# Performance work log

Measured on AMD Instinct MI355X. Metric: run time of the kernel, lower is better.

Reference implementation:

```python
import jax, jax.numpy as jnp
import numpy as np

NUM_NODES = 12
NUM_EDGES = 30
OUT_CH = 32
HID = 192
B = 8192
FEAT = 2 * (NUM_NODES - 1)            # 22
N = B * NUM_NODES                      # 98304 nodes
E = B * NUM_EDGES                      # 245760 edges
OUT_SPACE = NUM_NODES ** 2 - NUM_NODES # 132


def setup_inputs() -> dict:
    key = jax.random.key(0)
    ks = jax.random.split(key, 16)
    def p(k, shape, fan):
        return jax.random.normal(k, shape, dtype=jnp.float32) / np.float32(np.sqrt(fan))
    return {
        "x": jax.random.normal(ks[0], (N, FEAT), dtype=jnp.float32),
        "edge_attr": jax.random.normal(ks[1], (E, NUM_EDGES), dtype=jnp.float32),
        "edge_index": jax.random.randint(ks[2], (2, E), 0, N, dtype=jnp.int64) if jax.config.jax_enable_x64 else jax.random.randint(ks[2], (2, E), 0, N, dtype=jnp.int32),
        "mlp1_w1": p(ks[3], (NUM_EDGES, HID), NUM_EDGES),
        "mlp1_b1": jnp.zeros((HID,), jnp.float32),
        "mlp1_w2": p(ks[4], (HID, FEAT * OUT_CH), HID),
        "mlp1_b2": jnp.zeros((FEAT * OUT_CH,), jnp.float32),
        "root1": p(ks[5], (FEAT, OUT_CH), FEAT),
        "bias1": jnp.zeros((OUT_CH,), jnp.float32),
        "lin1_w": p(ks[6], (NUM_NODES * OUT_CH, 96), NUM_NODES * OUT_CH),
        "lin1_b": jnp.zeros((96,), jnp.float32),
        "lin2_w": p(ks[7], (96, 48), 96),
        "lin2_b": jnp.zeros((48,), jnp.float32),
        "lin3_w": p(ks[8], (48, OUT_SPACE), 48),
        "lin3_b": jnp.zeros((OUT_SPACE,), jnp.float32),
    }


def reference(x, edge_attr, edge_index, mlp1_w1, mlp1_b1, mlp1_w2, mlp1_b2,
              root1, bias1, lin1_w, lin1_b, lin2_w, lin2_b, lin3_w, lin3_b):
    src, dst = edge_index[0], edge_index[1]
    # Edge-MLP ('Understanding'): produces a [FEAT, OUT_CH] weight per edge
    h = jax.nn.relu(edge_attr @ mlp1_w1 + mlp1_b1)               # [E, HID]
    W = (h @ mlp1_w2 + mlp1_b2).reshape(-1, FEAT, OUT_CH)        # [E, 22, 32]
    # NNConv: gather source features, per-edge matmul, scatter-add to dst
    msg = jnp.einsum('ec,eco->eo', x[src], W)                    # [E, 32]
    agg = jax.ops.segment_sum(msg, dst, num_segments=x.shape[0]) # [N, 32]
    g = jax.nn.relu(x @ root1 + agg + bias1)                     # conv1 + ReLU
    # Dense head
    g = g.reshape(-1, NUM_NODES * OUT_CH)                        # [B, 384]
    g = jax.nn.relu(g @ lin1_w + lin1_b)
    g = jax.nn.relu(g @ lin2_w + lin2_b)
    g = jax.nn.relu(g @ lin3_w + lin3_b)                         # [B, 132]
    return g
```

## Files before the change

kernel.cpp:

```cpp
#include <hip/hip_runtime.h>
#include <hip/hip_bf16.h>

typedef short s8v __attribute__((ext_vector_type(8)));
typedef float f4v __attribute__((ext_vector_type(4)));

#define MFMA16(A,B,C) __builtin_amdgcn_mfma_f32_16x16x32_bf16((A),(B),(C),0,0,0)

#define E_TOT 245760
#define N_TOT 98304

__device__ __forceinline__ unsigned short f2bf(float f) {
    unsigned u = __builtin_bit_cast(unsigned, f);
    u += 0x7fffu + ((u >> 16) & 1u);
    return (unsigned short)(u >> 16);
}
__device__ __forceinline__ float bflo(unsigned u) {
    return __builtin_bit_cast(float, u << 16);
}
__device__ __forceinline__ float bfhi(unsigned u) {
    return __builtin_bit_cast(float, u & 0xffff0000u);
}
__device__ __forceinline__ void gload_lds16(const void* g, void* l) {
    __builtin_amdgcn_global_load_lds(
        (const __attribute__((address_space(1))) void*)g,
        (__attribute__((address_space(3))) void*)l, 16, 0, 0);
}

__global__ void pack_kernel(const float* __restrict__ w1, const float* __restrict__ w2,
                            const float* __restrict__ l1w, const float* __restrict__ l2w,
                            const float* __restrict__ l3w,
                            unsigned short* __restrict__ w1p, unsigned short* __restrict__ w2p,
                            unsigned short* __restrict__ l1p, unsigned short* __restrict__ l2p,
                            unsigned short* __restrict__ l3p)
{
    int idx = blockIdx.x * 256 + threadIdx.x;
    if (idx >= 192000) return;
    if (idx < 6144) {
        int i = idx & 7, l = (idx >> 3) & 63, nt = idx >> 9;
        int k = (l >> 4) * 8 + i, col = nt * 16 + (l & 15);
        w1p[idx] = f2bf(k < 30 ? w1[k * 192 + col] : 0.f);
    } else if (idx < 141312) {
        int e = idx - 6144;
        int i = e & 7, l = (e >> 3) & 63, rest = e >> 9;
        int s = rest % 6, ct = rest / 6, t = ct & 1, c = ct >> 1;
        int k = s * 32 + (l >> 4) * 8 + i, j = c * 32 + t * 16 + (l & 15);
        w2p[e] = f2bf(w2[k * 704 + j]);
    } else if (idx < 178176) {
        int e = idx - 141312;
        int i = e & 7, l = (e >> 3) & 63, rest = e >> 9;
        int s = rest % 12, nt = rest / 12;
        int k = s * 32 + (l >> 4) * 8 + i, j = nt * 16 + (l & 15);
        l1p[e] = f2bf(l1w[k * 96 + j]);
    } else if (idx < 182784) {
        int e = idx - 178176;
        int i = e & 7, l = (e >> 3) & 63, rest = e >> 9;
        int s = rest % 3, nt = rest / 3;
        int k = s * 32 + (l >> 4) * 8 + i, j = nt * 16 + (l & 15);
        l2p[e] = f2bf(l2w[k * 48 + j]);
    } else {
        int e = idx - 182784;
        int i = e & 7, l = (e >> 3) & 63, rest = e >> 9;
        int s = rest & 1, nt = rest >> 1;
        int k = s * 32 + (l >> 4) * 8 + i, j = nt * 16 + (l & 15);
        l3p[e] = f2bf((k < 48 && j < 132) ? l3w[k * 132 + j] : 0.f);
    }
}

__launch_bounds__(256, 3)
__global__ void edge_kernel(const float* __restrict__ x,
                            const float* __restrict__ ea,
                            const int*   __restrict__ eidx,
                            const unsigned short* __restrict__ w1p,
                            const unsigned short* __restrict__ w2p,
                            const float* __restrict__ b1,
                            const float* __restrict__ b2,
                            float* __restrict__ agg)
{
    __shared__ __align__(16) unsigned char smem[38400];
    unsigned short* w2u  = (unsigned short*)smem;
    unsigned short* hscr = (unsigned short*)smem;
    unsigned short* xs   = (unsigned short*)(smem + 25600);
    float*          b2l  = (float*)(smem + 34816);
    int*            dstl = (int*)(smem + 37632);

    const int tid  = threadIdx.x;
    const int wave = tid >> 6, lane = tid & 63;
    const int hi = lane >> 4, col = lane & 15;
    const int e0 = blockIdx.x * 192;

    for (int idx = tid; idx < 192 * 22; idx += 256) {
        int e = idx / 22, c = idx - e * 22;
        int s = eidx[e0 + e];
        xs[e * 24 + c] = f2bf(x[s * 22 + c]);
    }
    for (int idx = tid; idx < 192; idx += 256) dstl[idx] = eidx[E_TOT + e0 + idx];
    for (int idx = tid; idx < 704; idx += 256) b2l[idx] = b2[idx];

    s8v w1f[12];
#pragma unroll
    for (int nt = 0; nt < 12; ++nt) w1f[nt] = *(const s8v*)(w1p + (nt * 64 + lane) * 8);
    float b1v[12];
#pragma unroll
    for (int nt = 0; nt < 12; ++nt) b1v[nt] = b1[nt * 16 + col];

    s8v haf[3][6];
#pragma unroll
    for (int mt = 0; mt < 3; ++mt) {
        int er = e0 + wave * 48 + mt * 16 + col;
        s8v af;
#pragma unroll
        for (int i = 0; i < 8; ++i) {
            int k = hi * 8 + i;
            af[i] = (short)f2bf(k < 30 ? ea[er * 30 + k] : 0.f);
        }
        f4v hc[12];
#pragma unroll
        for (int nt = 0; nt < 12; ++nt) {
            f4v z = {0.f, 0.f, 0.f, 0.f};
            hc[nt] = MFMA16(af, w1f[nt], z);
        }
#pragma unroll
        for (int nt = 0; nt < 12; ++nt)
#pragma unroll
            for (int r = 0; r < 4; ++r) {
                float v = hc[nt][r] + b1v[nt];
                v = v > 0.f ? v : 0.f;
                hscr[(wave * 16 + hi * 4 + r) * 200 + nt * 16 + col] = f2bf(v);
            }
#pragma unroll
        for (int s = 0; s < 6; ++s)
            haf[mt][s] = *(const s8v*)&hscr[(wave * 16 + col) * 200 + s * 32 + hi * 8];
    }

    __syncthreads();

#pragma unroll
    for (int r = 0; r < 3; ++r)
        gload_lds16(w2p + (r * 256 + tid) * 8, w2u + (r * 256 + wave * 64) * 8);
    __syncthreads();

    f4v msg[3][2];
#pragma unroll
    for (int mt = 0; mt < 3; ++mt)
#pragma unroll
        for (int t = 0; t < 2; ++t) msg[mt][t] = (f4v){0.f, 0.f, 0.f, 0.f};

    for (int cp = 0; cp < 11; ++cp) {
        {
            const int c = 2 * cp;
#pragma unroll
            for (int r = 0; r < 3; ++r)
                gload_lds16(w2p + (c + 1) * 6144 + (r * 256 + tid) * 8,
                            w2u + 6144 + (r * 256 + wave * 64) * 8);
            f4v pacc[3][2];
#pragma unroll
            for (int t = 0; t < 2; ++t) {
                float bv = b2l[c * 32 + t * 16 + col];
#pragma unroll
                for (int mt = 0; mt < 3; ++mt) pacc[mt][t] = (f4v){bv, bv, bv, bv};
#pragma unroll
                for (int s = 0; s < 6; ++s) {
                    s8v bfr = *(const s8v*)&w2u[((t * 6 + s) * 64 + lane) * 8];
#pragma unroll
                    for (int mt = 0; mt < 3; ++mt)
                        pacc[mt][t] = MFMA16(haf[mt][s], bfr, pacc[mt][t]);
                }
            }
#pragma unroll
            for (int mt = 0; mt < 3; ++mt)
#pragma unroll
                for (int r = 0; r < 4; ++r) {
                    unsigned xu = *(const unsigned*)&xs[(wave * 48 + mt * 16 + hi * 4 + r) * 24 + c];
                    float xv = bflo(xu);
                    msg[mt][0][r] += xv * pacc[mt][0][r];
                    msg[mt][1][r] += xv * pacc[mt][1][r];
                }
            __syncthreads();
        }
        {
            const int c = 2 * cp + 1;
            if (c < 21) {
#pragma unroll
                for (int r = 0; r < 3; ++r)
                    gload_lds16(w2p + (c + 1) * 6144 + (r * 256 + tid) * 8,
                                w2u + (r * 256 + wave * 64) * 8);
            }
            f4v pacc[3][2];
#pragma unroll
            for (int t = 0; t < 2; ++t) {
                float bv = b2l[c * 32 + t * 16 + col];
#pragma unroll
                for (int mt = 0; mt < 3; ++mt) pacc[mt][t] = (f4v){bv, bv, bv, bv};
#pragma unroll
                for (int s = 0; s < 6; ++s) {
                    s8v bfr = *(const s8v*)&w2u[6144 + ((t * 6 + s) * 64 + lane) * 8];
#pragma unroll
                    for (int mt = 0; mt < 3; ++mt)
                        pacc[mt][t] = MFMA16(haf[mt][s], bfr, pacc[mt][t]);
                }
            }
#pragma unroll
            for (int mt = 0; mt < 3; ++mt)
#pragma unroll
                for (int r = 0; r < 4; ++r) {
                    unsigned xu = *(const unsigned*)&xs[(wave * 48 + mt * 16 + hi * 4 + r) * 24 + c - 1];
                    float xv = bfhi(xu);
                    msg[mt][0][r] += xv * pacc[mt][0][r];
                    msg[mt][1][r] += xv * pacc[mt][1][r];
                }
            __syncthreads();
        }
    }

#pragma unroll
    for (int mt = 0; mt < 3; ++mt)
#pragma unroll
        for (int r = 0; r < 4; ++r) {
            int e = wave * 48 + mt * 16 + hi * 4 + r;
            int d = dstl[e];
            atomicAdd(&agg[d * 32 + col],      msg[mt][0][r]);
            atomicAdd(&agg[d * 32 + 16 + col], msg[mt][1][r]);
        }
}

__launch_bounds__(256)
__global__ void node_kernel(const float* __restrict__ x, const float* __restrict__ agg,
                            const float* __restrict__ root1, const float* __restrict__ bias1,
                            unsigned short* __restrict__ g2d)
{
    const int tid = threadIdx.x, wave = tid >> 6, lane = tid & 63;
    const int hi = lane >> 4, col = lane & 15;
    const int n0 = blockIdx.x * 256 + wave * 64;

    s8v bfr[2];
#pragma unroll
    for (int nt = 0; nt < 2; ++nt)
#pragma unroll
        for (int i = 0; i < 8; ++i) {
            int k = hi * 8 + i;
            bfr[nt][i] = (short)f2bf(k < 22 ? root1[k * 32 + nt * 16 + col] : 0.f);
        }
    float bb0 = bias1[col], bb1 = bias1[16 + col];

#pragma unroll
    for (int mt = 0; mt < 4; ++mt) {
        int node = n0 + mt * 16 + col;
        s8v af;
        if (hi < 2) {
            const float2* p = (const float2*)&x[node * 22 + hi * 8];
            float2 t0 = p[0], t1 = p[1], t2 = p[2], t3 = p[3];
            af[0] = (short)f2bf(t0.x); af[1] = (short)f2bf(t0.y);
            af[2] = (short)f2bf(t1.x); af[3] = (short)f2bf(t1.y);
            af[4] = (short)f2bf(t2.x); af[5] = (short)f2bf(t2.y);
            af[6] = (short)f2bf(t3.x); af[7] = (short)f2bf(t3.y);
        } else if (hi == 2) {
            const float2* p = (const float2*)&x[node * 22 + 16];
            float2 t0 = p[0], t1 = p[1], t2 = p[2];
            af[0] = (short)f2bf(t0.x); af[1] = (short)f2bf(t0.y);
            af[2] = (short)f2bf(t1.x); af[3] = (short)f2bf(t1.y);
            af[4] = (short)f2bf(t2.x); af[5] = (short)f2bf(t2.y);
            af[6] = 0; af[7] = 0;
        } else {
            af = (s8v)0;
        }
        f4v c0 = {bb0, bb0, bb0, bb0};
        f4v c1 = {bb1, bb1, bb1, bb1};
        c0 = MFMA16(af, bfr[0], c0);
        c1 = MFMA16(af, bfr[1], c1);
#pragma unroll
        for (int r = 0; r < 4; ++r) {
            int row = n0 + mt * 16 + hi * 4 + r;
            float v0 = c0[r] + agg[row * 32 + col];
            float v1 = c1[r] + agg[row * 32 + 16 + col];
            g2d[row * 32 + col]      = f2bf(v0 > 0.f ? v0 : 0.f);
            g2d[row * 32 + 16 + col] = f2bf(v1 > 0.f ? v1 : 0.f);
        }
    }
}

__launch_bounds__(256)
__global__ void head_kernel(const unsigned short* __restrict__ g2d,
                            const unsigned short* __restrict__ l1p,
                            const unsigned short* __restrict__ l2p,
                            const unsigned short* __restrict__ l3p,
                            const float* __restrict__ l1b,
                            const float* __restrict__ l2b,
                            const float* __restrict__ l3b,
                            float* __restrict__ out)
{
    __shared__ __align__(16) unsigned short a1s[4][16][104];
    __shared__ __align__(16) unsigned short a2s[4][16][56];

    const int tid = threadIdx.x, wave = tid >> 6, lane = tid & 63;
    const int hi = lane >> 4, col = lane & 15;
    const int r0 = blockIdx.x * 64 + wave * 16;

    f4v acc1[6];
#pragma unroll
    for (int nt = 0; nt < 6; ++nt) {
        float bv = l1b[nt * 16 + col];
        acc1[nt] = (f4v){bv, bv, bv, bv};
    }
#pragma unroll
    for (int s = 0; s < 12; ++s) {
        s8v a = *(const s8v*)&g2d[(r0 + col) * 384 + s * 32 + hi * 8];
#pragma unroll
        for (int nt = 0; nt < 6; ++nt) {
            s8v b = *(const s8v*)&l1p[((nt * 12 + s) * 64 + lane) * 8];
            acc1[nt] = MFMA16(a, b, acc1[nt]);
        }
    }
#pragma unroll
    for (int nt = 0; nt < 6; ++nt)
#pragma unroll
        for (int r = 0; r < 4; ++r) {
            float v = acc1[nt][r];
            a1s[wave][hi * 4 + r][nt * 16 + col] = f2bf(v > 0.f ? v : 0.f);
        }

    f4v acc2[3];
#pragma unroll
    for (int nt = 0; nt < 3; ++nt) {
        float bv = l2b[nt * 16 + col];
        acc2[nt] = (f4v){bv, bv, bv, bv};
    }
#pragma unroll
    for (int s = 0; s < 3; ++s) {
        s8v a = *(const s8v*)&a1s[wave][col][s * 32 + hi * 8];
#pragma unroll
        for (int nt = 0; nt < 3; ++nt) {
            s8v b = *(const s8v*)&l2p[((nt * 3 + s) * 64 + lane) * 8];
            acc2[nt] = MFMA16(a, b, acc2[nt]);
        }
    }
#pragma unroll
    for (int nt = 0; nt < 3; ++nt)
#pragma unroll
        for (int r = 0; r < 4; ++r) {
            float v = acc2[nt][r];
            a2s[wave][hi * 4 + r][nt * 16 + col] = f2bf(v > 0.f ? v : 0.f);
        }

    f4v acc3[9];
#pragma unroll
    for (int nt = 0; nt < 9; ++nt) {
        int oc = nt * 16 + col;
        float bv = oc < 132 ? l3b[oc] : 0.f;
        acc3[nt] = (f4v){bv, bv, bv, bv};
    }
#pragma unroll
    for (int s = 0; s < 2; ++s) {
        s8v a;
        if (s == 1 && hi >= 2) a = (s8v)0;
        else a = *(const s8v*)&a2s[wave][col][s * 32 + hi * 8];
#pragma unroll
        for (int nt = 0; nt < 9; ++nt) {
            s8v b = *(const s8v*)&l3p[((nt * 2 + s) * 64 + lane) * 8];
            acc3[nt] = MFMA16(a, b, acc3[nt]);
        }
    }
#pragma unroll
    for (int nt = 0; nt < 9; ++nt) {
        int oc = nt * 16 + col;
        if (oc < 132) {
#pragma unroll
            for (int r = 0; r < 4; ++r) {
                float v = acc3[nt][r];
                out[(r0 + hi * 4 + r) * 132 + oc] = v > 0.f ? v : 0.f;
            }
        }
    }
}

extern "C" void kernel_launch(void* const* d_in, const int* in_sizes, int n_in,
                              void* d_out, int out_size, void* d_ws, size_t ws_size,
                              hipStream_t stream)
{
    const float* x     = (const float*)d_in[0];
    const float* ea    = (const float*)d_in[1];
    const int*   ei    = (const int*)d_in[2];
    const float* w1    = (const float*)d_in[3];
    const float* b1    = (const float*)d_in[4];
    const float* w2    = (const float*)d_in[5];
    const float* b2    = (const float*)d_in[6];
    const float* root1 = (const float*)d_in[7];
    const float* bias1 = (const float*)d_in[8];
    const float* l1w   = (const float*)d_in[9];
    const float* l1b   = (const float*)d_in[10];
    const float* l2w   = (const float*)d_in[11];
    const float* l2b   = (const float*)d_in[12];
    const float* l3w   = (const float*)d_in[13];
    const float* l3b   = (const float*)d_in[14];
    float* out = (float*)d_out;

    char* ws = (char*)d_ws;
    unsigned short* w1p = (unsigned short*)(ws + 0);
    unsigned short* w2p = (unsigned short*)(ws + 12288);
    unsigned short* l1p = (unsigned short*)(ws + 282624);
    unsigned short* l2p = (unsigned short*)(ws + 356352);
    unsigned short* l3p = (unsigned short*)(ws + 365568);
    float*          agg = (float*)(ws + 384000);
    unsigned short* g2d = (unsigned short*)(ws + 12966912);

    hipMemsetAsync(agg, 0, (size_t)N_TOT * 32 * 4, stream);
    pack_kernel<<<750, 256, 0, stream>>>(w1, w2, l1w, l2w, l3w, w1p, w2p, l1p, l2p, l3p);
    edge_kernel<<<1280, 256, 0, stream>>>(x, ea, ei, w1p, w2p, b1, b2, agg);
    node_kernel<<<384, 256, 0, stream>>>(x, agg, root1, bias1, g2d);
    head_kernel<<<128, 256, 0, stream>>>(g2d, l1p, l2p, l3p, l1b, l2b, l3b, out);
}
```

Before: 214.4 us.

## Seed agg with root term, fuse node ReLU into head, read W2 from global

Measured after the change: 286.9 us. 1.34x slower.

```diff
diff --git a/kernel.cpp b/kernel.cpp
--- a/kernel.cpp
+++ b/kernel.cpp
@@ -19,11 +19,6 @@
 }
 __device__ __forceinline__ float bfhi(unsigned u) {
     return __builtin_bit_cast(float, u & 0xffff0000u);
-}
-__device__ __forceinline__ void gload_lds16(const void* g, void* l) {
-    __builtin_amdgcn_global_load_lds(
-        (const __attribute__((address_space(1))) void*)g,
-        (__attribute__((address_space(3))) void*)l, 16, 0, 0);
 }
 
 __global__ void pack_kernel(const float* __restrict__ w1, const float* __restrict__ w2,
@@ -41,22 +36,22 @@
         w1p[idx] = f2bf(k < 30 ? w1[k * 192 + col] : 0.f);
     } else if (idx < 141312) {
         int e = idx - 6144;
-        int i = e & 7, l = (e >> 3) & 63, rest = e >> 9;
-        int s = rest % 6, ct = rest / 6, t = ct & 1, c = ct >> 1;
-        int k = s * 32 + (l >> 4) * 8 + i, j = c * 32 + t * 16 + (l & 15);
-        w2p[e] = f2bf(w2[k * 704 + j]);
+        int k = e / 704, j = e - k * 704;
+        int c = j >> 5, t = (j >> 4) & 1, colv = j & 15;
+        int s = k >> 5, hi = (k >> 3) & 3, i = k & 7;
+        w2p[((c * 2 + t) * 6 + s) * 512 + (hi * 16 + colv) * 8 + i] = f2bf(w2[e]);
     } else if (idx < 178176) {
         int e = idx - 141312;
-        int i = e & 7, l = (e >> 3) & 63, rest = e >> 9;
-        int s = rest % 12, nt = rest / 12;
-        int k = s * 32 + (l >> 4) * 8 + i, j = nt * 16 + (l & 15);
-        l1p[e] = f2bf(l1w[k * 96 + j]);
+        int k = e / 96, j = e - k * 96;
+        int s = k >> 5, hi = (k >> 3) & 3, i = k & 7;
+        int nt = j >> 4, colv = j & 15;
+        l1p[(nt * 12 + s) * 512 + (hi * 16 + colv) * 8 + i] = f2bf(l1w[e]);
     } else if (idx < 182784) {
         int e = idx - 178176;
-        int i = e & 7, l = (e >> 3) & 63, rest = e >> 9;
-        int s = rest % 3, nt = rest / 3;
-        int k = s * 32 + (l >> 4) * 8 + i, j = nt * 16 + (l & 15);
-        l2p[e] = f2bf(l2w[k * 48 + j]);
+        int k = e / 48, j = e - k * 48;
+        int s = k >> 5, hi = (k >> 3) & 3, i = k & 7;
+        int nt = j >> 4, colv = j & 15;
+        l2p[(nt * 3 + s) * 512 + (hi * 16 + colv) * 8 + i] = f2bf(l2w[e]);
     } else {
         int e = idx - 182784;
         int i = e & 7, l = (e >> 3) & 63, rest = e >> 9;
@@ -66,167 +61,9 @@
     }
 }
 
-__launch_bounds__(256, 3)
-__global__ void edge_kernel(const float* __restrict__ x,
-                            const float* __restrict__ ea,
-                            const int*   __restrict__ eidx,
-                            const unsigned short* __restrict__ w1p,
-                            const unsigned short* __restrict__ w2p,
-                            const float* __restrict__ b1,
-                            const float* __restrict__ b2,
-                            float* __restrict__ agg)
-{
-    __shared__ __align__(16) unsigned char smem[38400];
-    unsigned short* w2u  = (unsigned short*)smem;
-    unsigned short* hscr = (unsigned short*)smem;
-    unsigned short* xs   = (unsigned short*)(smem + 25600);
-    float*          b2l  = (float*)(smem + 34816);
-    int*            dstl = (int*)(smem + 37632);
-
-    const int tid  = threadIdx.x;
-    const int wave = tid >> 6, lane = tid & 63;
-    const int hi = lane >> 4, col = lane & 15;
-    const int e0 = blockIdx.x * 192;
-
-    for (int idx = tid; idx < 192 * 22; idx += 256) {
-        int e = idx / 22, c = idx - e * 22;
-        int s = eidx[e0 + e];
-        xs[e * 24 + c] = f2bf(x[s * 22 + c]);
-    }
-    for (int idx = tid; idx < 192; idx += 256) dstl[idx] = eidx[E_TOT + e0 + idx];
-    for (int idx = tid; idx < 704; idx += 256) b2l[idx] = b2[idx];
-
-    s8v w1f[12];
-#pragma unroll
-    for (int nt = 0; nt < 12; ++nt) w1f[nt] = *(const s8v*)(w1p + (nt * 64 + lane) * 8);
-    float b1v[12];
-#pragma unroll
-    for (int nt = 0; nt < 12; ++nt) b1v[nt] = b1[nt * 16 + col];
-
-    s8v haf[3][6];
-#pragma unroll
-    for (int mt = 0; mt < 3; ++mt) {
-        int er = e0 + wave * 48 + mt * 16 + col;
-        s8v af;
-#pragma unroll
-        for (int i = 0; i < 8; ++i) {
-            int k = hi * 8 + i;
-            af[i] = (short)f2bf(k < 30 ? ea[er * 30 + k] : 0.f);
-        }
-        f4v hc[12];
-#pragma unroll
-        for (int nt = 0; nt < 12; ++nt) {
-            f4v z = {0.f, 0.f, 0.f, 0.f};
-            hc[nt] = MFMA16(af, w1f[nt], z);
-        }
-#pragma unroll
-        for (int nt = 0; nt < 12; ++nt)
-#pragma unroll
-            for (int r = 0; r < 4; ++r) {
-                float v = hc[nt][r] + b1v[nt];
-                v = v > 0.f ? v : 0.f;
-                hscr[(wave * 16 + hi * 4 + r) * 200 + nt * 16 + col] = f2bf(v);
-            }
-#pragma unroll
-        for (int s = 0; s < 6; ++s)
-            haf[mt][s] = *(const s8v*)&hscr[(wave * 16 + col) * 200 + s * 32 + hi * 8];
-    }
-
-    __syncthreads();
-
-#pragma unroll
-    for (int r = 0; r < 3; ++r)
-        gload_lds16(w2p + (r * 256 + tid) * 8, w2u + (r * 256 + wave * 64) * 8);
-    __syncthreads();
-
-    f4v msg[3][2];
-#pragma unroll
-    for (int mt = 0; mt < 3; ++mt)
-#pragma unroll
-        for (int t = 0; t < 2; ++t) msg[mt][t] = (f4v){0.f, 0.f, 0.f, 0.f};
-
-    for (int cp = 0; cp < 11; ++cp) {
-        {
-            const int c = 2 * cp;
-#pragma unroll
-            for (int r = 0; r < 3; ++r)
-                gload_lds16(w2p + (c + 1) * 6144 + (r * 256 + tid) * 8,
-                            w2u + 6144 + (r * 256 + wave * 64) * 8);
-            f4v pacc[3][2];
-#pragma unroll
-            for (int t = 0; t < 2; ++t) {
-                float bv = b2l[c * 32 + t * 16 + col];
-#pragma unroll
-                for (int mt = 0; mt < 3; ++mt) pacc[mt][t] = (f4v){bv, bv, bv, bv};
-#pragma unroll
-                for (int s = 0; s < 6; ++s) {
-                    s8v bfr = *(const s8v*)&w2u[((t * 6 + s) * 64 + lane) * 8];
-#pragma unroll
-                    for (int mt = 0; mt < 3; ++mt)
-                        pacc[mt][t] = MFMA16(haf[mt][s], bfr, pacc[mt][t]);
-                }
-            }
-#pragma unroll
-            for (int mt = 0; mt < 3; ++mt)
-#pragma unroll
-                for (int r = 0; r < 4; ++r) {
-                    unsigned xu = *(const unsigned*)&xs[(wave * 48 + mt * 16 + hi * 4 + r) * 24 + c];
-                    float xv = bflo(xu);
-                    msg[mt][0][r] += xv * pacc[mt][0][r];
-                    msg[mt][1][r] += xv * pacc[mt][1][r];
-                }
-            __syncthreads();
-        }
-        {
-            const int c = 2 * cp + 1;
-            if (c < 21) {
-#pragma unroll
-                for (int r = 0; r < 3; ++r)
-                    gload_lds16(w2p + (c + 1) * 6144 + (r * 256 + tid) * 8,
-                                w2u + (r * 256 + wave * 64) * 8);
-            }
-            f4v pacc[3][2];
-#pragma unroll
-            for (int t = 0; t < 2; ++t) {
-                float bv = b2l[c * 32 + t * 16 + col];
-#pragma unroll
-                for (int mt = 0; mt < 3; ++mt) pacc[mt][t] = (f4v){bv, bv, bv, bv};
-#pragma unroll
-                for (int s = 0; s < 6; ++s) {
-                    s8v bfr = *(const s8v*)&w2u[6144 + ((t * 6 + s) * 64 + lane) * 8];
-#pragma unroll
-                    for (int mt = 0; mt < 3; ++mt)
-                        pacc[mt][t] = MFMA16(haf[mt][s], bfr, pacc[mt][t]);
-                }
-            }
-#pragma unroll
-            for (int mt = 0; mt < 3; ++mt)
-#pragma unroll
-                for (int r = 0; r < 4; ++r) {
-                    unsigned xu = *(const unsigned*)&xs[(wave * 48 + mt * 16 + hi * 4 + r) * 24 + c - 1];
-                    float xv = bfhi(xu);
-                    msg[mt][0][r] += xv * pacc[mt][0][r];
-                    msg[mt][1][r] += xv * pacc[mt][1][r];
-                }
-            __syncthreads();
-        }
-    }
-
-#pragma unroll
-    for (int mt = 0; mt < 3; ++mt)
-#pragma unroll
-        for (int r = 0; r < 4; ++r) {
-            int e = wave * 48 + mt * 16 + hi * 4 + r;
-            int d = dstl[e];
-            atomicAdd(&agg[d * 32 + col],      msg[mt][0][r]);
-            atomicAdd(&agg[d * 32 + 16 + col], msg[mt][1][r]);
-        }
-}
-
 __launch_bounds__(256)
-__global__ void node_kernel(const float* __restrict__ x, const float* __restrict__ agg,
-                            const float* __restrict__ root1, const float* __restrict__ bias1,
-                            unsigned short* __restrict__ g2d)
+__global__ void init_kernel(const float* __restrict__ x, const float* __restrict__ root1,
+                            const float* __restrict__ bias1, float* __restrict__ agg)
 {
     const int tid = threadIdx.x, wave = tid >> 6, lane = tid & 63;
     const int hi = lane >> 4, col = lane & 15;
@@ -270,16 +107,141 @@
 #pragma unroll
         for (int r = 0; r < 4; ++r) {
             int row = n0 + mt * 16 + hi * 4 + r;
-            float v0 = c0[r] + agg[row * 32 + col];
-            float v1 = c1[r] + agg[row * 32 + 16 + col];
-            g2d[row * 32 + col]      = f2bf(v0 > 0.f ? v0 : 0.f);
-            g2d[row * 32 + 16 + col] = f2bf(v1 > 0.f ? v1 : 0.f);
-        }
-    }
-}
-
-__launch_bounds__(256)
-__global__ void head_kernel(const unsigned short* __restrict__ g2d,
+            agg[row * 32 + col]      = c0[r];
+            agg[row * 32 + 16 + col] = c1[r];
+        }
+    }
+}
+
+__launch_bounds__(256, 3)
+__global__ void edge_kernel(const float* __restrict__ x,
+                            const float* __restrict__ ea,
+                            const int*   __restrict__ eidx,
+                            const unsigned short* __restrict__ w1p,
+                            const unsigned short* __restrict__ w2p,
+                            const float* __restrict__ b1,
+                            const float* __restrict__ b2,
+                            float* __restrict__ agg)
+{
+    __shared__ __align__(16) unsigned char smem[37632];
+    unsigned short* hscr = (unsigned short*)smem;
+    unsigned short* xs   = (unsigned short*)(smem + 25600);
+    float*          b2l  = (float*)(smem + 34048);
+    int*            dstl = (int*)(smem + 36864);
+
+    const int tid  = threadIdx.x;
+    const int wave = tid >> 6, lane = tid & 63;
+    const int hi = lane >> 4, col = lane & 15;
+    const int e0 = blockIdx.x * 192;
+
+    if (tid < 192) {
+        int s = eidx[e0 + tid];
+        dstl[tid] = eidx[E_TOT + e0 + tid];
+        const float2* p = (const float2*)&x[s * 22];
+#pragma unroll
+        for (int c2 = 0; c2 < 11; ++c2) {
+            float2 v = p[c2];
+            unsigned pk = (unsigned)f2bf(v.x) | ((unsigned)f2bf(v.y) << 16);
+            *(unsigned*)&xs[tid * 22 + 2 * c2] = pk;
+        }
+    }
+    for (int idx = tid; idx < 704; idx += 256) b2l[idx] = b2[idx];
+
+    s8v w1f[12];
+#pragma unroll
+    for (int nt = 0; nt < 12; ++nt) w1f[nt] = *(const s8v*)(w1p + (nt * 64 + lane) * 8);
+    float b1v[12];
+#pragma unroll
+    for (int nt = 0; nt < 12; ++nt) b1v[nt] = b1[nt * 16 + col];
+
+    s8v haf[3][6];
+#pragma unroll
+    for (int mt = 0; mt < 3; ++mt) {
+        int er = e0 + wave * 48 + mt * 16 + col;
+        s8v af;
+#pragma unroll
+        for (int i = 0; i < 8; ++i) {
+            int k = hi * 8 + i;
+            af[i] = (short)f2bf(k < 30 ? ea[er * 30 + k] : 0.f);
+        }
+        f4v hc[12];
+#pragma unroll
+        for (int nt = 0; nt < 12; ++nt) {
+            f4v z = {0.f, 0.f, 0.f, 0.f};
+            hc[nt] = MFMA16(af, w1f[nt], z);
+        }
+#pragma unroll
+        for (int nt = 0; nt < 12; ++nt)
+#pragma unroll
+            for (int r = 0; r < 4; ++r) {
+                float v = hc[nt][r] + b1v[nt];
+                v = v > 0.f ? v : 0.f;
+                hscr[(wave * 16 + hi * 4 + r) * 200 + nt * 16 + col] = f2bf(v);
+            }
+#pragma unroll
+        for (int s = 0; s < 6; ++s)
+            haf[mt][s] = *(const s8v*)&hscr[(wave * 16 + col) * 200 + s * 32 + hi * 8];
+    }
+
+    __syncthreads();
+
+    f4v msg[3][2];
+#pragma unroll
+    for (int mt = 0; mt < 3; ++mt)
+#pragma unroll
+        for (int t = 0; t < 2; ++t) msg[mt][t] = (f4v){0.f, 0.f, 0.f, 0.f};
+
+    for (int cp = 0; cp < 11; ++cp) {
+        unsigned xu[12];
+#pragma unroll
+        for (int mt = 0; mt < 3; ++mt)
+#pragma unroll
+            for (int r = 0; r < 4; ++r)
+                xu[mt * 4 + r] = *(const unsigned*)&xs[(wave * 48 + mt * 16 + hi * 4 + r) * 22 + 2 * cp];
+
+#pragma unroll
+        for (int sub = 0; sub < 2; ++sub) {
+            const int c = 2 * cp + sub;
+            f4v pacc[3][2];
+#pragma unroll
+            for (int t = 0; t < 2; ++t) {
+                s8v bfr[6];
+#pragma unroll
+                for (int s = 0; s < 6; ++s)
+                    bfr[s] = *(const s8v*)&w2p[c * 6144 + ((t * 6 + s) * 64 + lane) * 8];
+                float bv = b2l[c * 32 + t * 16 + col];
+#pragma unroll
+                for (int mt = 0; mt < 3; ++mt) pacc[mt][t] = (f4v){bv, bv, bv, bv};
+#pragma unroll
+                for (int s = 0; s < 6; ++s)
+#pragma unroll
+                    for (int mt = 0; mt < 3; ++mt)
+                        pacc[mt][t] = MFMA16(haf[mt][s], bfr[s], pacc[mt][t]);
+            }
+#pragma unroll
+            for (int mt = 0; mt < 3; ++mt)
+#pragma unroll
+                for (int r = 0; r < 4; ++r) {
+                    float xv = sub ? bfhi(xu[mt * 4 + r]) : bflo(xu[mt * 4 + r]);
+                    msg[mt][0][r] += xv * pacc[mt][0][r];
+                    msg[mt][1][r] += xv * pacc[mt][1][r];
+                }
+        }
+    }
+
+#pragma unroll
+    for (int mt = 0; mt < 3; ++mt)
+#pragma unroll
+        for (int r = 0; r < 4; ++r) {
+            int e = wave * 48 + mt * 16 + hi * 4 + r;
+            int d = dstl[e];
+            atomicAdd(&agg[d * 32 + col],      msg[mt][0][r]);
+            atomicAdd(&agg[d * 32 + 16 + col], msg[mt][1][r]);
+        }
+}
+
+__launch_bounds__(64)
+__global__ void head_kernel(const float* __restrict__ agg,
                             const unsigned short* __restrict__ l1p,
                             const unsigned short* __restrict__ l2p,
                             const unsigned short* __restrict__ l3p,
@@ -288,12 +250,27 @@
                             const float* __restrict__ l3b,
                             float* __restrict__ out)
 {
-    __shared__ __align__(16) unsigned short a1s[4][16][104];
-    __shared__ __align__(16) unsigned short a2s[4][16][56];
-
-    const int tid = threadIdx.x, wave = tid >> 6, lane = tid & 63;
+    __shared__ __align__(16) unsigned short gls[16 * 392];
+    __shared__ __align__(16) unsigned short a1s[16 * 104];
+    __shared__ __align__(16) unsigned short a2s[16 * 56];
+
+    const int lane = threadIdx.x & 63;
     const int hi = lane >> 4, col = lane & 15;
-    const int r0 = blockIdx.x * 64 + wave * 16;
+    const int r0 = blockIdx.x * 16;
+
+    const f4v* a4 = (const f4v*)(agg + (size_t)r0 * 384);
+#pragma unroll
+    for (int it = 0; it < 24; ++it) {
+        int q = it * 64 + lane;
+        f4v v = a4[q];
+#pragma unroll
+        for (int j = 0; j < 4; ++j) v[j] = v[j] > 0.f ? v[j] : 0.f;
+        int row = q / 96, coloff = (q - row * 96) * 4;
+        unsigned pk0 = (unsigned)f2bf(v[0]) | ((unsigned)f2bf(v[1]) << 16);
+        unsigned pk1 = (unsigned)f2bf(v[2]) | ((unsigned)f2bf(v[3]) << 16);
+        *(unsigned*)&gls[row * 392 + coloff]     = pk0;
+        *(unsigned*)&gls[row * 392 + coloff + 2] = pk1;
+    }
 
     f4v acc1[6];
 #pragma unroll
@@ -303,7 +280,7 @@
     }
 #pragma unroll
     for (int s = 0; s < 12; ++s) {
-        s8v a = *(const s8v*)&g2d[(r0 + col) * 384 + s * 32 + hi * 8];
+        s8v a = *(const s8v*)&gls[col * 392 + s * 32 + hi * 8];
 #pragma unroll
         for (int nt = 0; nt < 6; ++nt) {
             s8v b = *(const s8v*)&l1p[((nt * 12 + s) * 64 + lane) * 8];
@@ -315,7 +292,7 @@
 #pragma unroll
         for (int r = 0; r < 4; ++r) {
             float v = acc1[nt][r];
-            a1s[wave][hi * 4 + r][nt * 16 + col] = f2bf(v > 0.f ? v : 0.f);
+            a1s[(hi * 4 + r) * 104 + nt * 16 + col] = f2bf(v > 0.f ? v : 0.f);
         }
 
     f4v acc2[3];
@@ -326,7 +303,7 @@
     }
 #pragma unroll
     for (int s = 0; s < 3; ++s) {
-        s8v a = *(const s8v*)&a1s[wave][col][s * 32 + hi * 8];
+        s8v a = *(const s8v*)&a1s[col * 104 + s * 32 + hi * 8];
 #pragma unroll
         for (int nt = 0; nt < 3; ++nt) {
             s8v b = *(const s8v*)&l2p[((nt * 3 + s) * 64 + lane) * 8];
@@ -338,7 +315,7 @@
 #pragma unroll
         for (int r = 0; r < 4; ++r) {
             float v = acc2[nt][r];
-            a2s[wave][hi * 4 + r][nt * 16 + col] = f2bf(v > 0.f ? v : 0.f);
+            a2s[(hi * 4 + r) * 56 + nt * 16 + col] = f2bf(v > 0.f ? v : 0.f);
         }
 
     f4v acc3[9];
@@ -352,7 +329,7 @@
     for (int s = 0; s < 2; ++s) {
         s8v a;
         if (s == 1 && hi >= 2) a = (s8v)0;
-        else a = *(const s8v*)&a2s[wave][col][s * 32 + hi * 8];
+        else a = *(const s8v*)&a2s[col * 56 + s * 32 + hi * 8];
 #pragma unroll
         for (int nt = 0; nt < 9; ++nt) {
             s8v b = *(const s8v*)&l3p[((nt * 2 + s) * 64 + lane) * 8];
@@ -400,11 +377,9 @@
     unsigned short* l2p = (unsigned short*)(ws + 356352);
     unsigned short* l3p = (unsigned short*)(ws + 365568);
     float*          agg = (float*)(ws + 384000);
-    unsigned short* g2d = (unsigned short*)(ws + 12966912);
-
-    hipMemsetAsync(agg, 0, (size_t)N_TOT * 32 * 4, stream);
+
     pack_kernel<<<750, 256, 0, stream>>>(w1, w2, l1w, l2w, l3w, w1p, w2p, l1p, l2p, l3p);
+    init_kernel<<<384, 256, 0, stream>>>(x, root1, bias1, agg);
     edge_kernel<<<1280, 256, 0, stream>>>(x, ea, ei, w1p, w2p, b1, b2, agg);
-    node_kernel<<<384, 256, 0, stream>>>(x, agg, root1, bias1, g2d);
-    head_kernel<<<128, 256, 0, stream>>>(g2d, l1p, l2p, l3p, l1b, l2b, l3b, out);
-}
+    head_kernel<<<512, 64, 0, stream>>>(agg, l1p, l2p, l3p, l1b, l2b, l3b, out);
+}
```

## Triple-buffer w2 chunks in edge kernel and fuse node+head kernels

Applied to the files above, without the earlier changes.

Result: slower. 232.6 us (+8.5%).

```diff
diff --git a/kernel.cpp b/kernel.cpp
--- a/kernel.cpp
+++ b/kernel.cpp
@@ -8,6 +8,10 @@
 
 #define E_TOT 245760
 #define N_TOT 98304
+
+#define VM_WAIT3 asm volatile("s_waitcnt vmcnt(3)" ::: "memory")
+#define VM_WAIT0 asm volatile("s_waitcnt vmcnt(0)" ::: "memory")
+#define SBAR     __builtin_amdgcn_s_barrier()
 
 __device__ __forceinline__ unsigned short f2bf(float f) {
     unsigned u = __builtin_bit_cast(unsigned, f);
@@ -26,7 +30,8 @@
         (__attribute__((address_space(3))) void*)l, 16, 0, 0);
 }
 
-__global__ void pack_kernel(const float* __restrict__ w1, const float* __restrict__ w2,
+__launch_bounds__(256)
+__global__ void prep_kernel(const float* __restrict__ w1, const float* __restrict__ w2,
                             const float* __restrict__ l1w, const float* __restrict__ l2w,
                             const float* __restrict__ l3w,
                             unsigned short* __restrict__ w1p, unsigned short* __restrict__ w2p,
@@ -76,24 +81,29 @@
                             const float* __restrict__ b2,
                             float* __restrict__ agg)
 {
-    __shared__ __align__(16) unsigned char smem[38400];
-    unsigned short* w2u  = (unsigned short*)smem;
+    __shared__ __align__(16) unsigned char smem[48896];
+    unsigned short* w2c  = (unsigned short*)smem;
     unsigned short* hscr = (unsigned short*)smem;
-    unsigned short* xs   = (unsigned short*)(smem + 25600);
-    float*          b2l  = (float*)(smem + 34816);
-    int*            dstl = (int*)(smem + 37632);
+    unsigned short* xs   = (unsigned short*)(smem + 36864);
+    float*          b2l  = (float*)(smem + 45312);
+    int*            dstl = (int*)(smem + 48128);
 
     const int tid  = threadIdx.x;
     const int wave = tid >> 6, lane = tid & 63;
     const int hi = lane >> 4, col = lane & 15;
     const int e0 = blockIdx.x * 192;
 
-    for (int idx = tid; idx < 192 * 22; idx += 256) {
-        int e = idx / 22, c = idx - e * 22;
-        int s = eidx[e0 + e];
-        xs[e * 24 + c] = f2bf(x[s * 22 + c]);
-    }
-    for (int idx = tid; idx < 192; idx += 256) dstl[idx] = eidx[E_TOT + e0 + idx];
+    if (tid < 192) {
+        int s = eidx[e0 + tid];
+        dstl[tid] = eidx[E_TOT + e0 + tid];
+        const float2* p = (const float2*)&x[s * 22];
+#pragma unroll
+        for (int c2 = 0; c2 < 11; ++c2) {
+            float2 v = p[c2];
+            unsigned pk = (unsigned)f2bf(v.x) | ((unsigned)f2bf(v.y) << 16);
+            *(unsigned*)&xs[tid * 22 + 2 * c2] = pk;
+        }
+    }
     for (int idx = tid; idx < 704; idx += 256) b2l[idx] = b2[idx];
 
     s8v w1f[12];
@@ -136,8 +146,10 @@
 
 #pragma unroll
     for (int r = 0; r < 3; ++r)
-        gload_lds16(w2p + (r * 256 + tid) * 8, w2u + (r * 256 + wave * 64) * 8);
-    __syncthreads();
+        gload_lds16(w2p + (r * 256 + tid) * 8, w2c + (r * 256 + wave * 64) * 8);
+#pragma unroll
+    for (int r = 0; r < 3; ++r)
+        gload_lds16(w2p + 6144 + (r * 256 + tid) * 8, w2c + 6144 + (r * 256 + wave * 64) * 8);
 
     f4v msg[3][2];
 #pragma unroll
@@ -145,13 +157,29 @@
 #pragma unroll
         for (int t = 0; t < 2; ++t) msg[mt][t] = (f4v){0.f, 0.f, 0.f, 0.f};
 
+    int bufA = 0;
     for (int cp = 0; cp < 11; ++cp) {
+        unsigned xu[12];
+#pragma unroll
+        for (int mt = 0; mt < 3; ++mt)
+#pragma unroll
+            for (int r = 0; r < 4; ++r)
+                xu[mt * 4 + r] = *(const unsigned*)&xs[(wave * 48 + mt * 16 + hi * 4 + r) * 22 + 2 * cp];
+
         {
             const int c = 2 * cp;
-#pragma unroll
-            for (int r = 0; r < 3; ++r)
-                gload_lds16(w2p + (c + 1) * 6144 + (r * 256 + tid) * 8,
-                            w2u + 6144 + (r * 256 + wave * 64) * 8);
+            VM_WAIT3;
+            SBAR;
+            if (cp < 10) {
+                const int nb = bufA;
+                const int dst = (bufA + 2) % 3;
+#pragma unroll
+                for (int r = 0; r < 3; ++r)
+                    gload_lds16(w2p + (c + 2) * 6144 + (r * 256 + tid) * 8,
+                                w2c + dst * 6144 + (r * 256 + wave * 64) * 8);
+                (void)nb;
+            }
+            const int base = bufA * 6144;
             f4v pacc[3][2];
 #pragma unroll
             for (int t = 0; t < 2; ++t) {
@@ -160,7 +188,7 @@
                 for (int mt = 0; mt < 3; ++mt) pacc[mt][t] = (f4v){bv, bv, bv, bv};
 #pragma unroll
                 for (int s = 0; s < 6; ++s) {
-                    s8v bfr = *(const s8v*)&w2u[((t * 6 + s) * 64 + lane) * 8];
+                    s8v bfr = *(const s8v*)&w2c[base + ((t * 6 + s) * 64 + lane) * 8];
 #pragma unroll
                     for (int mt = 0; mt < 3; ++mt)
                         pacc[mt][t] = MFMA16(haf[mt][s], bfr, pacc[mt][t]);
@@ -170,21 +198,23 @@
             for (int mt = 0; mt < 3; ++mt)
 #pragma unroll
                 for (int r = 0; r < 4; ++r) {
-                    unsigned xu = *(const unsigned*)&xs[(wave * 48 + mt * 16 + hi * 4 + r) * 24 + c];
-                    float xv = bflo(xu);
+                    float xv = bflo(xu[mt * 4 + r]);
                     msg[mt][0][r] += xv * pacc[mt][0][r];
                     msg[mt][1][r] += xv * pacc[mt][1][r];
                 }
-            __syncthreads();
         }
         {
             const int c = 2 * cp + 1;
-            if (c < 21) {
+            if (cp < 10) { VM_WAIT3; } else { VM_WAIT0; }
+            SBAR;
+            if (cp < 10) {
+                const int dst = bufA;
 #pragma unroll
                 for (int r = 0; r < 3; ++r)
-                    gload_lds16(w2p + (c + 1) * 6144 + (r * 256 + tid) * 8,
-                                w2u + (r * 256 + wave * 64) * 8);
-            }
+                    gload_lds16(w2p + (c + 2) * 6144 + (r * 256 + tid) * 8,
+                                w2c + dst * 6144 + (r * 256 + wave * 64) * 8);
+            }
+            const int base = ((bufA + 1) % 3) * 6144;
             f4v pacc[3][2];
 #pragma unroll
             for (int t = 0; t < 2; ++t) {
@@ -193,7 +223,7 @@
                 for (int mt = 0; mt < 3; ++mt) pacc[mt][t] = (f4v){bv, bv, bv, bv};
 #pragma unroll
                 for (int s = 0; s < 6; ++s) {
-                    s8v bfr = *(const s8v*)&w2u[6144 + ((t * 6 + s) * 64 + lane) * 8];
+                    s8v bfr = *(const s8v*)&w2c[base + ((t * 6 + s) * 64 + lane) * 8];
 #pragma unroll
                     for (int mt = 0; mt < 3; ++mt)
                         pacc[mt][t] = MFMA16(haf[mt][s], bfr, pacc[mt][t]);
@@ -203,13 +233,12 @@
             for (int mt = 0; mt < 3; ++mt)
 #pragma unroll
                 for (int r = 0; r < 4; ++r) {
-                    unsigned xu = *(const unsigned*)&xs[(wave * 48 + mt * 16 + hi * 4 + r) * 24 + c - 1];
-                    float xv = bfhi(xu);
+                    float xv = bfhi(xu[mt * 4 + r]);
                     msg[mt][0][r] += xv * pacc[mt][0][r];
                     msg[mt][1][r] += xv * pacc[mt][1][r];
                 }
-            __syncthreads();
-        }
+        }
+        bufA = (bufA + 2) % 3;
     }
 
 #pragma unroll
@@ -224,13 +253,26 @@
 }
 
 __launch_bounds__(256)
-__global__ void node_kernel(const float* __restrict__ x, const float* __restrict__ agg,
-                            const float* __restrict__ root1, const float* __restrict__ bias1,
-                            unsigned short* __restrict__ g2d)
+__global__ void head_kernel(const float* __restrict__ x,
+                            const float* __restrict__ agg,
+                            const float* __restrict__ root1,
+                            const float* __restrict__ bias1,
+                            const unsigned short* __restrict__ l1p,
+                            const unsigned short* __restrict__ l2p,
+                            const unsigned short* __restrict__ l3p,
+                            const float* __restrict__ l1b,
+                            const float* __restrict__ l2b,
+                            const float* __restrict__ l3b,
+                            float* __restrict__ out)
 {
+    __shared__ __align__(16) unsigned short gls[4 * 8 * 392];
+    __shared__ __align__(16) unsigned short a1s[4 * 8 * 104];
+    __shared__ __align__(16) unsigned short a2s[4 * 8 * 56];
+
     const int tid = threadIdx.x, wave = tid >> 6, lane = tid & 63;
-    const int hi = lane >> 4, col = lane & 15;
-    const int n0 = blockIdx.x * 256 + wave * 64;
+    const int hi = lane >> 4, col = lane & 15, c8 = col & 7;
+    const int g0 = blockIdx.x * 32 + wave * 8;
+    const int n0 = g0 * 12;
 
     s8v bfr[2];
 #pragma unroll
@@ -243,7 +285,7 @@
     float bb0 = bias1[col], bb1 = bias1[16 + col];
 
 #pragma unroll
-    for (int mt = 0; mt < 4; ++mt) {
+    for (int mt = 0; mt < 6; ++mt) {
         int node = n0 + mt * 16 + col;
         s8v af;
         if (hi < 2) {
@@ -269,31 +311,15 @@
         c1 = MFMA16(af, bfr[1], c1);
 #pragma unroll
         for (int r = 0; r < 4; ++r) {
-            int row = n0 + mt * 16 + hi * 4 + r;
+            int ln = mt * 16 + hi * 4 + r;
+            int g = ln / 12, nig = ln - g * 12;
+            int row = n0 + ln;
             float v0 = c0[r] + agg[row * 32 + col];
             float v1 = c1[r] + agg[row * 32 + 16 + col];
-            g2d[row * 32 + col]      = f2bf(v0 > 0.f ? v0 : 0.f);
-            g2d[row * 32 + 16 + col] = f2bf(v1 > 0.f ? v1 : 0.f);
-        }
-    }
-}
-
-__launch_bounds__(256)
-__global__ void head_kernel(const unsigned short* __restrict__ g2d,
-                            const unsigned short* __restrict__ l1p,
-                            const unsigned short* __restrict__ l2p,
-                            const unsigned short* __restrict__ l3p,
-                            const float* __restrict__ l1b,
-                            const float* __restrict__ l2b,
-                            const float* __restrict__ l3b,
-                            float* __restrict__ out)
-{
-    __shared__ __align__(16) unsigned short a1s[4][16][104];
-    __shared__ __align__(16) unsigned short a2s[4][16][56];
-
-    const int tid = threadIdx.x, wave = tid >> 6, lane = tid & 63;
-    const int hi = lane >> 4, col = lane & 15;
-    const int r0 = blockIdx.x * 64 + wave * 16;
+            gls[(wave * 8 + g) * 392 + nig * 32 + col]      = f2bf(v0 > 0.f ? v0 : 0.f);
+            gls[(wave * 8 + g) * 392 + nig * 32 + 16 + col] = f2bf(v1 > 0.f ? v1 : 0.f);
+        }
+    }
 
     f4v acc1[6];
 #pragma unroll
@@ -303,20 +329,22 @@
     }
 #pragma unroll
     for (int s = 0; s < 12; ++s) {
-        s8v a = *(const s8v*)&g2d[(r0 + col) * 384 + s * 32 + hi * 8];
+        s8v a = *(const s8v*)&gls[(wave * 8 + c8) * 392 + s * 32 + hi * 8];
 #pragma unroll
         for (int nt = 0; nt < 6; ++nt) {
             s8v b = *(const s8v*)&l1p[((nt * 12 + s) * 64 + lane) * 8];
             acc1[nt] = MFMA16(a, b, acc1[nt]);
         }
     }
-#pragma unroll
-    for (int nt = 0; nt < 6; ++nt)
-#pragma unroll
-        for (int r = 0; r < 4; ++r) {
-            float v = acc1[nt][r];
-            a1s[wave][hi * 4 + r][nt * 16 + col] = f2bf(v > 0.f ? v : 0.f);
-        }
+    if (hi < 2) {
+#pragma unroll
+        for (int nt = 0; nt < 6; ++nt)
+#pragma unroll
+            for (int r = 0; r < 4; ++r) {
+                float v = acc1[nt][r];
+                a1s[(wave * 8 + hi * 4 + r) * 104 + nt * 16 + col] = f2bf(v > 0.f ? v : 0.f);
+            }
+    }
 
     f4v acc2[3];
 #pragma unroll
@@ -326,20 +354,22 @@
     }
 #pragma unroll
     for (int s = 0; s < 3; ++s) {
-        s8v a = *(const s8v*)&a1s[wave][col][s * 32 + hi * 8];
+        s8v a = *(const s8v*)&a1s[(wave * 8 + c8) * 104 + s * 32 + hi * 8];
 #pragma unroll
         for (int nt = 0; nt < 3; ++nt) {
             s8v b = *(const s8v*)&l2p[((nt * 3 + s) * 64 + lane) * 8];
             acc2[nt] = MFMA16(a, b, acc2[nt]);
         }
     }
-#pragma unroll
-    for (int nt = 0; nt < 3; ++nt)
-#pragma unroll
-        for (int r = 0; r < 4; ++r) {
-            float v = acc2[nt][r];
-            a2s[wave][hi * 4 + r][nt * 16 + col] = f2bf(v > 0.f ? v : 0.f);
-        }
+    if (hi < 2) {
+#pragma unroll
+        for (int nt = 0; nt < 3; ++nt)
+#pragma unroll
+            for (int r = 0; r < 4; ++r) {
+                float v = acc2[nt][r];
+                a2s[(wave * 8 + hi * 4 + r) * 56 + nt * 16 + col] = f2bf(v > 0.f ? v : 0.f);
+            }
+    }
 
     f4v acc3[9];
 #pragma unroll
@@ -352,21 +382,23 @@
     for (int s = 0; s < 2; ++s) {
         s8v a;
         if (s == 1 && hi >= 2) a = (s8v)0;
-        else a = *(const s8v*)&a2s[wave][col][s * 32 + hi * 8];
+        else a = *(const s8v*)&a2s[(wave * 8 + c8) * 56 + s * 32 + hi * 8];
 #pragma unroll
         for (int nt = 0; nt < 9; ++nt) {
             s8v b = *(const s8v*)&l3p[((nt * 2 + s) * 64 + lane) * 8];
             acc3[nt] = MFMA16(a, b, acc3[nt]);
         }
     }
-#pragma unroll
-    for (int nt = 0; nt < 9; ++nt) {
-        int oc = nt * 16 + col;
-        if (oc < 132) {
-#pragma unroll
-            for (int r = 0; r < 4; ++r) {
-                float v = acc3[nt][r];
-                out[(r0 + hi * 4 + r) * 132 + oc] = v > 0.f ? v : 0.f;
+    if (hi < 2) {
+#pragma unroll
+        for (int nt = 0; nt < 9; ++nt) {
+            int oc = nt * 16 + col;
+            if (oc < 132) {
+#pragma unroll
+                for (int r = 0; r < 4; ++r) {
+                    float v = acc3[nt][r];
+                    out[(g0 + hi * 4 + r) * 132 + oc] = v > 0.f ? v : 0.f;
+                }
             }
         }
     }
@@ -400,11 +432,10 @@
     unsigned short* l2p = (unsigned short*)(ws + 356352);
     unsigned short* l3p = (unsigned short*)(ws + 365568);
     float*          agg = (float*)(ws + 384000);
-    unsigned short* g2d = (unsigned short*)(ws + 12966912);
 
     hipMemsetAsync(agg, 0, (size_t)N_TOT * 32 * 4, stream);
-    pack_kernel<<<750, 256, 0, stream>>>(w1, w2, l1w, l2w, l3w, w1p, w2p, l1p, l2p, l3p);
+    prep_kernel<<<750, 256, 0, stream>>>(w1, w2, l1w, l2w, l3w, w1p, w2p, l1p, l2p, l3p);
     edge_kernel<<<1280, 256, 0, stream>>>(x, ea, ei, w1p, w2p, b1, b2, agg);
-    node_kernel<<<384, 256, 0, stream>>>(x, agg, root1, bias1, g2d);
-    head_kernel<<<128, 256, 0, stream>>>(g2d, l1p, l2p, l3p, l1b, l2b, l3b, out);
-}
+    head_kernel<<<256, 256, 0, stream>>>(x, agg, root1, bias1, l1p, l2p, l3p,
+                                         l1b, l2b, l3b, out);
+}
```
